# Performance work log

Hardware: AMD Instinct MI355X
Metric: run time of the kernel (lower is better)

The kernel has to match this reference:

```python
import jax, jax.numpy as jnp
import numpy as np

NUM_EXPERTS = 8
TOP_K = 2
BALANCE_LOSS_COEF = 0.01


def setup_inputs() -> dict:
    key = jax.random.key(0)
    ks = jax.random.split(key, 5)
    B, S, H, I, E = 8, 2048, 512, 2048, NUM_EXPERTS
    return {
        "hidden_states": jax.random.normal(ks[0], (B, S, H), dtype=jnp.float32),
        "Wg": jax.random.normal(ks[1], (H, E), dtype=jnp.float32) * (1.0 / np.sqrt(H)),
        "bg": jnp.zeros((E,), dtype=jnp.float32),
        "W1": jax.random.normal(ks[2], (E, H, I), dtype=jnp.float32) * (1.0 / np.sqrt(H)),
        "b1": jnp.zeros((E, I), dtype=jnp.float32),
        "W2": jax.random.normal(ks[3], (E, I, H), dtype=jnp.float32) * (1.0 / np.sqrt(I)),
        "b2": jnp.zeros((E, H), dtype=jnp.float32),
    }


def reference(hidden_states, Wg, bg, W1, b1, W2, b2):
    B, S, H = hidden_states.shape
    E, K = NUM_EXPERTS, TOP_K

    # ---- Router: softmax gate + top-k, renormalized weights ----
    logits = jnp.einsum('bsh,he->bse', hidden_states, Wg) + bg       # [B,S,E]
    probs = jax.nn.softmax(logits, axis=-1)                          # [B,S,E]
    top_p, top_i = jax.lax.top_k(probs, K)                           # [B,S,K]
    routing_weights = top_p / jnp.sum(top_p, axis=-1, keepdims=True)  # [B,S,K]

    # ---- Experts: compute every expert densely (small fixed E), then gather ----
    h = jnp.einsum('bsh,ehi->ebsi', hidden_states, W1) + b1[:, None, None, :]
    h = jax.nn.gelu(h)
    y = jnp.einsum('ebsi,eih->ebsh', h, W2) + b2[:, None, None, :]   # [E,B,S,H]

    y = jnp.moveaxis(y, 0, 2)                                        # [B,S,E,H]
    sel = jnp.take_along_axis(y, top_i[..., None], axis=2)           # [B,S,K,H]
    output = jnp.sum(routing_weights[..., None] * sel, axis=2) + hidden_states

    # ---- Load balancing loss (Switch-style): E * sum_e f_e * P_e ----
    assign = jnp.sum(jax.nn.one_hot(top_i, E, dtype=probs.dtype), axis=2)  # [B,S,E]
    f = jnp.mean(assign, axis=(0, 1)) / K                            # fraction dispatched
    P = jnp.mean(probs, axis=(0, 1))                                 # mean router prob
    balance_loss = BALANCE_LOSS_COEF * E * jnp.sum(f * P)

    return output, balance_loss
```

## Files before the change

kernel.cpp:

```cpp
#include <hip/hip_runtime.h>

#define BS_TOK 16384
#define HD 512
#define IDIM 2048
#define NE 8
#define RT_MAX 264
#define CAP (RT_MAX * 128)

typedef unsigned short u16;
typedef unsigned int u32;
typedef __attribute__((ext_vector_type(8))) __bf16 bf16x8;
typedef __attribute__((ext_vector_type(4))) float f32x4;

__device__ __forceinline__ u16 f2bf(float f) {
  u32 u = __builtin_bit_cast(u32, f);
  u += 0x7fffu + ((u >> 16) & 1u);
  return (u16)(u >> 16);
}
__device__ __forceinline__ float bflo(u32 u) { return __builtin_bit_cast(float, u << 16); }
__device__ __forceinline__ float bfhi(u32 u) { return __builtin_bit_cast(float, u & 0xffff0000u); }
__device__ __forceinline__ float gelu_t(float v) {
  float c = 0.7978845608028654f * (v + 0.044715f * v * v * v);
  return v / (1.0f + __expf(-2.0f * c));
}
__device__ __forceinline__ void gload16(const u16* g, u16* l) {
  __builtin_amdgcn_global_load_lds((const __attribute__((address_space(1))) u16*)g,
                                   (__attribute__((address_space(3))) u16*)l, 16, 0, 0);
}

__global__ void k_init(u32* counts, u32* pos, float* Psum, int* perm_t, float* perm_w) {
  int i = blockIdx.x * 256 + threadIdx.x;
  if (i < NE) { counts[i] = 0; pos[i] = 0; Psum[i] = 0.f; }
  if (i < CAP) { perm_t[i] = 0; perm_w[i] = 0.f; }
}

__global__ void k_transpose2(const float* __restrict__ W1, u16* __restrict__ W1T,
                             const float* __restrict__ W2, u16* __restrict__ W2T) {
  __shared__ float t[32][33];
  int z = blockIdx.z;
  const float* in; u16* out; int R, C, bx, by;
  if (z < NE) { in = W1; out = W1T; R = HD; C = IDIM; bx = blockIdx.x; by = blockIdx.y; }
  else { in = W2; out = W2T; R = IDIM; C = HD; bx = blockIdx.y; by = blockIdx.x; z -= NE; }
  size_t eb = (size_t)z * HD * IDIM;
  int c0 = bx * 32, r0 = by * 32;
  int tx = threadIdx.x, ty = threadIdx.y;
  #pragma unroll
  for (int j = ty; j < 32; j += 8) t[j][tx] = in[eb + (size_t)(r0 + j) * C + (c0 + tx)];
  __syncthreads();
  #pragma unroll
  for (int j = ty; j < 32; j += 8) out[eb + (size_t)(c0 + j) * R + (r0 + tx)] = f2bf(t[tx][j]);
}

__global__ void k_router(const float* __restrict__ x, const float* __restrict__ Wg,
                         const float* __restrict__ bg, int* __restrict__ top_e,
                         float* __restrict__ top_w, u32* __restrict__ counts,
                         float* __restrict__ Psum, u16* __restrict__ xb) {
  __shared__ float wg_s[HD * NE];
  __shared__ float Pp[NE];
  __shared__ u32 cnt[NE];
  int tid = threadIdx.x;
  if (tid < NE) { Pp[tid] = 0.f; cnt[tid] = 0; }
  for (int i = tid; i < HD * NE; i += 256) wg_s[i] = Wg[i];
  __syncthreads();
  int wv = tid >> 6, lane = tid & 63;
  int t = blockIdx.x * 4 + wv;
  const float4* xr = (const float4*)(x + (size_t)t * HD + lane * 8);
  float4 a = xr[0], b = xr[1];
  u32 p0 = f2bf(a.x) | ((u32)f2bf(a.y) << 16);
  u32 p1 = f2bf(a.z) | ((u32)f2bf(a.w) << 16);
  u32 p2 = f2bf(b.x) | ((u32)f2bf(b.y) << 16);
  u32 p3 = f2bf(b.z) | ((u32)f2bf(b.w) << 16);
  ((uint4*)(xb + (size_t)t * HD))[lane] = make_uint4(p0, p1, p2, p3);

  float acc[NE];
  #pragma unroll
  for (int e = 0; e < NE; ++e) acc[e] = 0.f;
  #pragma unroll
  for (int j = 0; j < 8; ++j) {
    float xv = j < 4 ? (&a.x)[j] : (&b.x)[j - 4];
    int h = lane * 8 + j;
    #pragma unroll
    for (int e = 0; e < NE; ++e) acc[e] += xv * wg_s[h * NE + e];
  }
  #pragma unroll
  for (int off = 32; off > 0; off >>= 1) {
    #pragma unroll
    for (int e = 0; e < NE; ++e) acc[e] += __shfl_down(acc[e], off);
  }
  if (lane == 0) {
    float lg[NE];
    #pragma unroll
    for (int e = 0; e < NE; ++e) lg[e] = acc[e] + bg[e];
    int i1 = 0; float m1 = lg[0];
    #pragma unroll
    for (int e = 1; e < NE; ++e) if (lg[e] > m1) { m1 = lg[e]; i1 = e; }
    int i2 = -1; float m2 = -1e30f;
    #pragma unroll
    for (int e = 0; e < NE; ++e) if (e != i1 && lg[e] > m2) { m2 = lg[e]; i2 = e; }
    float s = 0.f, p[NE];
    #pragma unroll
    for (int e = 0; e < NE; ++e) { p[e] = __expf(lg[e] - m1); s += p[e]; }
    float inv = 1.f / s;
    #pragma unroll
    for (int e = 0; e < NE; ++e) { p[e] *= inv; atomicAdd(&Pp[e], p[e]); }
    float denom = p[i1] + p[i2];
    top_e[2 * t] = i1; top_e[2 * t + 1] = i2;
    top_w[2 * t] = p[i1] / denom; top_w[2 * t + 1] = p[i2] / denom;
    atomicAdd(&cnt[i1], 1u); atomicAdd(&cnt[i2], 1u);
  }
  __syncthreads();
  if (tid < NE) { atomicAdd(&counts[tid], cnt[tid]); atomicAdd(&Psum[tid], Pp[tid]); }
}

__global__ void k_scan(const u32* __restrict__ counts, const float* __restrict__ Psum,
                       u32* __restrict__ padoff, u32* __restrict__ pos, float* __restrict__ out) {
  if (threadIdx.x == 0) {
    u32 off = 0; float loss = 0.f;
    for (int e = 0; e < NE; ++e) {
      padoff[e] = off; pos[e] = off;
      off += ((counts[e] + 127u) / 128u) * 128u;
      loss += ((float)counts[e] / (float)(BS_TOK * 2)) * (Psum[e] / (float)BS_TOK);
    }
    padoff[NE] = off;
    out[(size_t)BS_TOK * HD] = 0.01f * (float)NE * loss;
  }
}

__global__ void k_scatter(const int* __restrict__ top_e, const float* __restrict__ top_w,
                          u32* __restrict__ pos, int* __restrict__ perm_t,
                          float* __restrict__ perm_w, int* __restrict__ inv) {
  int g = blockIdx.x * 256 + threadIdx.x;
  int e = top_e[g]; float wgt = top_w[g];
  int lane = threadIdx.x & 63;
  #pragma unroll
  for (int ee = 0; ee < NE; ++ee) {
    unsigned long long m = __ballot(e == ee);
    if (e == ee) {
      int nb = __popcll(m & ((1ull << lane) - 1ull));
      int leader = __ffsll((unsigned long long)m) - 1;
      u32 base = 0;
      if (lane == leader) base = atomicAdd(&pos[ee], (u32)__popcll(m));
      base = __shfl(base, leader);
      int slot = (int)base + nb;
      perm_t[slot] = g >> 1;
      perm_w[slot] = wgt;
      inv[g] = slot;
    }
  }
}

__global__ void k_outinit(const float* __restrict__ x, float* __restrict__ out) {
  size_t i = (size_t)blockIdx.x * 256 + threadIdx.x;
  ((float4*)out)[i] = ((const float4*)x)[i];
}

template <int KSTEPS, int NCT, int NTOT, bool GATHER, bool ACT, bool ATOMIC>
__global__ __launch_bounds__(256, 2) void k_gemm(
    const u16* __restrict__ A, int lda, const u16* __restrict__ W,
    const float* __restrict__ bias, const int* __restrict__ perm_t,
    const float* __restrict__ perm_w, const u32* __restrict__ padoff,
    u16* __restrict__ C, float* __restrict__ outA, int rt0) {
  __shared__ u16 As[2][8192], Bs[2][8192];
  int nb = gridDim.x;
  int b = blockIdx.x;
  int tile = (b & 7) * (nb >> 3) + (b >> 3);
  int rt = rt0 + tile / NCT, ct = tile % NCT;
  u32 s0 = (u32)rt * 128u;
  if (rt >= RT_MAX || s0 >= padoff[NE]) return;
  int e = 0;
  #pragma unroll
  for (int k = 1; k < NE; ++k) e += (s0 >= padoff[k]) ? 1 : 0;

  int tid = threadIdx.x;
  int wv = tid >> 6, lane = tid & 63;
  int l15 = lane & 15, lg4 = lane >> 4;
  int wr = wv >> 1, wc = wv & 1;

  int srow = tid >> 3;
  int cb = (tid & 7) * 16;
  int cbs = (cb ^ ((srow & 7) << 4)) >> 1;

  const u16* ap[4]; const u16* bp[4];
  #pragma unroll
  for (int i = 0; i < 4; ++i) {
    int r = i * 32 + srow;
    int arow = GATHER ? perm_t[s0 + r] : (int)(s0 + r);
    ap[i] = A + (size_t)arow * lda + cbs;
    bp[i] = W + ((size_t)e * NTOT + ct * 128 + r) * (KSTEPS * 64) + cbs;
  }

  f32x4 acc[4][4] = {};

  #pragma unroll
  for (int i = 0; i < 4; ++i) gload16(ap[i], As[0] + tid * 8 + i * 2048);
  #pragma unroll
  for (int i = 0; i < 4; ++i) gload16(bp[i], Bs[0] + tid * 8 + i * 2048);
  #pragma unroll
  for (int i = 0; i < 4; ++i) gload16(ap[i] + 64, As[1] + tid * 8 + i * 2048);
  #pragma unroll
  for (int i = 0; i < 4; ++i) gload16(bp[i] + 64, Bs[1] + tid * 8 + i * 2048);
  asm volatile("s_waitcnt vmcnt(8)" ::: "memory");
  __builtin_amdgcn_sched_barrier(0);
  __builtin_amdgcn_s_barrier();

  for (int ks = 0; ks < KSTEPS; ++ks) {
    int cur = ks & 1;
    const u16* Ab = As[cur];
    const u16* Bb = Bs[cur];
    bf16x8 af[2][4], bf[2][4];
    #pragma unroll
    for (int kk = 0; kk < 2; ++kk) {
      #pragma unroll
      for (int f = 0; f < 4; ++f) {
        int ra = wr * 64 + f * 16 + l15;
        af[kk][f] = *(const bf16x8*)((const char*)Ab +
                    (ra * 128 + ((kk * 64 + lg4 * 16) ^ ((ra & 7) << 4))));
        int rb = wc * 64 + f * 16 + l15;
        bf[kk][f] = *(const bf16x8*)((const char*)Bb +
                    (rb * 128 + ((kk * 64 + lg4 * 16) ^ ((rb & 7) << 4))));
      }
    }
    asm volatile("s_waitcnt lgkmcnt(0)" ::: "memory");
    __builtin_amdgcn_sched_barrier(0);
    __builtin_amdgcn_s_barrier();

    if (ks + 2 < KSTEPS) {
      int k0 = (ks + 2) * 64;
      #pragma unroll
      for (int i = 0; i < 4; ++i) gload16(ap[i] + k0, As[cur] + tid * 8 + i * 2048);
      #pragma unroll
      for (int i = 0; i < 4; ++i) gload16(bp[i] + k0, Bs[cur] + tid * 8 + i * 2048);
    }

    __builtin_amdgcn_s_setprio(1);
    #pragma unroll
    for (int kk = 0; kk < 2; ++kk) {
      #pragma unroll
      for (int i = 0; i < 4; ++i)
        #pragma unroll
        for (int j = 0; j < 4; ++j)
          acc[i][j] = __builtin_amdgcn_mfma_f32_16x16x32_bf16(af[kk][i], bf[kk][j], acc[i][j], 0, 0, 0);
    }
    __builtin_amdgcn_s_setprio(0);

    if (ks + 1 < KSTEPS) {
      if (ks + 2 < KSTEPS) {
        asm volatile("s_waitcnt vmcnt(8)" ::: "memory");
      } else {
        asm volatile("s_waitcnt vmcnt(0)" ::: "memory");
      }
      __builtin_amdgcn_sched_barrier(0);
      __builtin_amdgcn_s_barrier();
    }
  }

  int base_n = ct * 128 + wc * 64;
  float bv[4];
  #pragma unroll
  for (int j = 0; j < 4; ++j) bv[j] = bias[e * NTOT + base_n + j * 16 + l15];

  #pragma unroll
  for (int i = 0; i < 4; ++i) {
    u32 mrow = s0 + wr * 64 + i * 16 + lg4 * 4;
    #pragma unroll
    for (int rr = 0; rr < 4; ++rr) {
      u32 m = mrow + rr;
      if (ATOMIC) {
        int tok = perm_t[m]; float wt = perm_w[m];
        if (wt != 0.f) {
          #pragma unroll
          for (int j = 0; j < 4; ++j) {
            float v = (acc[i][j][rr] + bv[j]) * wt;
            atomicAdd(outA + (size_t)tok * HD + base_n + j * 16 + l15, v);
          }
        }
      } else {
        #pragma unroll
        for (int j = 0; j < 4; ++j) {
          float v = acc[i][j][rr] + bv[j];
          if (ACT) v = gelu_t(v);
          C[(size_t)m * NTOT + base_n + j * 16 + l15] = f2bf(v);
        }
      }
    }
  }
}

__global__ void k_final(const float* __restrict__ x, const u16* __restrict__ y,
                        const int* __restrict__ inv, const float* __restrict__ top_w,
                        float* __restrict__ out) {
  int tid = threadIdx.x;
  int t = blockIdx.x * 4 + (tid >> 6);
  int lane = tid & 63;
  int s0 = inv[2 * t], s1 = inv[2 * t + 1];
  float w0 = top_w[2 * t], w1 = top_w[2 * t + 1];
  size_t xo = (size_t)t * HD + lane * 8;
  float4 a = *(const float4*)(x + xo);
  float4 b = *(const float4*)(x + xo + 4);
  uint4 ya = *(const uint4*)(y + (size_t)s0 * HD + lane * 8);
  uint4 yb = *(const uint4*)(y + (size_t)s1 * HD + lane * 8);
  float4 o0, o1;
  o0.x = a.x + w0 * bflo(ya.x) + w1 * bflo(yb.x);
  o0.y = a.y + w0 * bfhi(ya.x) + w1 * bfhi(yb.x);
  o0.z = a.z + w0 * bflo(ya.y) + w1 * bflo(yb.y);
  o0.w = a.w + w0 * bfhi(ya.y) + w1 * bfhi(yb.y);
  o1.x = b.x + w0 * bflo(ya.z) + w1 * bflo(yb.z);
  o1.y = b.y + w0 * bfhi(ya.z) + w1 * bfhi(yb.z);
  o1.z = b.z + w0 * bflo(ya.w) + w1 * bflo(yb.w);
  o1.w = b.w + w0 * bfhi(ya.w) + w1 * bfhi(yb.w);
  *(float4*)(out + xo) = o0;
  *(float4*)(out + xo + 4) = o1;
}

extern "C" void kernel_launch(void* const* d_in, const int* in_sizes, int n_in,
                              void* d_out, int out_size, void* d_ws, size_t ws_size,
                              hipStream_t stream) {
  const float* x  = (const float*)d_in[0];
  const float* Wg = (const float*)d_in[1];
  const float* bg = (const float*)d_in[2];
  const float* W1 = (const float*)d_in[3];
  const float* b1 = (const float*)d_in[4];
  const float* W2 = (const float*)d_in[5];
  const float* b2 = (const float*)d_in[6];
  float* out = (float*)d_out;

  char* w = (char*)d_ws;
  u32* counts  = (u32*)(w + 0);
  u32* pos     = (u32*)(w + 32);
  float* Psum  = (float*)(w + 64);
  u32* padoff  = (u32*)(w + 96);
  int* top_e   = (int*)(w + 256);
  float* top_w = (float*)(w + 256 + 131072);
  int* invm    = (int*)(w + 256 + 2 * 131072);
  int* perm_t  = (int*)(w + 256 + 3 * 131072);
  float* perm_w = (float*)(w + 256 + 3 * 131072 + 135168);
  u16* xb  = (u16*)(w + 663808);
  u16* W1T = (u16*)(w + 17441024);
  u16* W2T = (u16*)(w + 34218240);
  u16* h   = (u16*)(w + 50995456);
  u16* y   = (u16*)(w + 189407488);

  bool modeA = ws_size >= 224010496ull;
  int T;
  if (modeA) {
    T = RT_MAX;
  } else {
    size_t hspace = ws_size > 50995456ull ? ws_size - 50995456ull : 0;
    T = (int)(hspace / (128ull * IDIM * 2));
    T &= ~1;
    if (T < 2) return;
    if (T > RT_MAX) T = RT_MAX;
  }

  k_init<<<(CAP + 255) / 256, 256, 0, stream>>>(counts, pos, Psum, perm_t, perm_w);
  k_transpose2<<<dim3(IDIM / 32, HD / 32, 2 * NE), dim3(32, 8), 0, stream>>>(W1, W1T, W2, W2T);
  k_router<<<BS_TOK / 4, 256, 0, stream>>>(x, Wg, bg, top_e, top_w, counts, Psum, xb);
  k_scan<<<1, 64, 0, stream>>>(counts, Psum, padoff, pos, out);
  k_scatter<<<(BS_TOK * 2) / 256, 256, 0, stream>>>(top_e, top_w, pos, perm_t, perm_w, invm);
  if (!modeA) k_outinit<<<(BS_TOK * HD / 4) / 256, 256, 0, stream>>>(x, out);

  int nch = (RT_MAX + T - 1) / T;
  for (int c = 0; c < nch; ++c) {
    int rt0 = c * T;
    u16* hadj = h - (size_t)rt0 * 128 * IDIM;
    k_gemm<8, 16, IDIM, true, true, false><<<T * 16, 256, 0, stream>>>(
        xb, HD, W1T, b1, perm_t, perm_w, padoff, hadj, nullptr, rt0);
    if (modeA) {
      k_gemm<32, 4, HD, false, false, false><<<T * 4, 256, 0, stream>>>(
          hadj, IDIM, W2T, b2, perm_t, perm_w, padoff, y, nullptr, rt0);
    } else {
      k_gemm<32, 4, HD, false, false, true><<<T * 4, 256, 0, stream>>>(
          hadj, IDIM, W2T, b2, perm_t, perm_w, padoff, nullptr, out, rt0);
    }
  }
  if (modeA) k_final<<<BS_TOK / 4, 256, 0, stream>>>(x, y, invm, top_w, out);
}
```

Measured before the change: 380.2 us.

## Use hardware bf16 convert, exp2-based GELU, bias-initialized accumulators, memset init

Replaces the software round-to-nearest bf16 conversion with the v_cvt_pk_bf16_f32 instruction in the weight transpose and GEMM epilogue. GELU is rewritten with a folded-constant exp2 and a hardware reciprocal. The bias is loaded into the accumulators before the K loop, so the epilogue no longer adds it. The k_init kernel is replaced by two hipMemsetAsync calls. Together these trim epilogue ALU work and one kernel launch, at some risk to rounding behaviour and to memset offsets matching the workspace layout.

```diff
diff --git a/kernel.cpp b/kernel.cpp
--- a/kernel.cpp
+++ b/kernel.cpp
@@ -17,21 +17,20 @@
   u += 0x7fffu + ((u >> 16) & 1u);
   return (u16)(u >> 16);
 }
+__device__ __forceinline__ u16 f2bf_hw(float f) {
+  u32 r;
+  asm("v_cvt_pk_bf16_f32 %0, %1, %2" : "=v"(r) : "v"(f), "v"(f));
+  return (u16)r;
+}
 __device__ __forceinline__ float bflo(u32 u) { return __builtin_bit_cast(float, u << 16); }
 __device__ __forceinline__ float bfhi(u32 u) { return __builtin_bit_cast(float, u & 0xffff0000u); }
 __device__ __forceinline__ float gelu_t(float v) {
-  float c = 0.7978845608028654f * (v + 0.044715f * v * v * v);
-  return v / (1.0f + __expf(-2.0f * c));
+  float t = v * (-2.302558f - 0.1029474f * v * v);
+  return v * __builtin_amdgcn_rcpf(1.0f + __builtin_amdgcn_exp2f(t));
 }
 __device__ __forceinline__ void gload16(const u16* g, u16* l) {
   __builtin_amdgcn_global_load_lds((const __attribute__((address_space(1))) u16*)g,
                                    (__attribute__((address_space(3))) u16*)l, 16, 0, 0);
-}
-
-__global__ void k_init(u32* counts, u32* pos, float* Psum, int* perm_t, float* perm_w) {
-  int i = blockIdx.x * 256 + threadIdx.x;
-  if (i < NE) { counts[i] = 0; pos[i] = 0; Psum[i] = 0.f; }
-  if (i < CAP) { perm_t[i] = 0; perm_w[i] = 0.f; }
 }
 
 __global__ void k_transpose2(const float* __restrict__ W1, u16* __restrict__ W1T,
@@ -48,7 +47,7 @@
   for (int j = ty; j < 32; j += 8) t[j][tx] = in[eb + (size_t)(r0 + j) * C + (c0 + tx)];
   __syncthreads();
   #pragma unroll
-  for (int j = ty; j < 32; j += 8) out[eb + (size_t)(c0 + j) * R + (r0 + tx)] = f2bf(t[tx][j]);
+  for (int j = ty; j < 32; j += 8) out[eb + (size_t)(c0 + j) * R + (r0 + tx)] = f2bf_hw(t[tx][j]);
 }
 
 __global__ void k_router(const float* __restrict__ x, const float* __restrict__ Wg,
@@ -189,7 +188,14 @@
     bp[i] = W + ((size_t)e * NTOT + ct * 128 + r) * (KSTEPS * 64) + cbs;
   }
 
-  f32x4 acc[4][4] = {};
+  int base_n = ct * 128 + wc * 64;
+  f32x4 acc[4][4];
+  #pragma unroll
+  for (int j = 0; j < 4; ++j) {
+    float bv = bias[e * NTOT + base_n + j * 16 + l15];
+    #pragma unroll
+    for (int i = 0; i < 4; ++i) acc[i][j] = f32x4{bv, bv, bv, bv};
+  }
 
   #pragma unroll
   for (int i = 0; i < 4; ++i) gload16(ap[i], As[0] + tid * 8 + i * 2048);
@@ -254,11 +260,6 @@
     }
   }
 
-  int base_n = ct * 128 + wc * 64;
-  float bv[4];
-  #pragma unroll
-  for (int j = 0; j < 4; ++j) bv[j] = bias[e * NTOT + base_n + j * 16 + l15];
-
   #pragma unroll
   for (int i = 0; i < 4; ++i) {
     u32 mrow = s0 + wr * 64 + i * 16 + lg4 * 4;
@@ -270,16 +271,16 @@
         if (wt != 0.f) {
           #pragma unroll
           for (int j = 0; j < 4; ++j) {
-            float v = (acc[i][j][rr] + bv[j]) * wt;
+            float v = acc[i][j][rr] * wt;
             atomicAdd(outA + (size_t)tok * HD + base_n + j * 16 + l15, v);
           }
         }
       } else {
         #pragma unroll
         for (int j = 0; j < 4; ++j) {
-          float v = acc[i][j][rr] + bv[j];
+          float v = acc[i][j][rr];
           if (ACT) v = gelu_t(v);
-          C[(size_t)m * NTOT + base_n + j * 16 + l15] = f2bf(v);
+          C[(size_t)m * NTOT + base_n + j * 16 + l15] = f2bf_hw(v);
         }
       }
     }
@@ -352,7 +353,8 @@
     if (T > RT_MAX) T = RT_MAX;
   }
 
-  k_init<<<(CAP + 255) / 256, 256, 0, stream>>>(counts, pos, Psum, perm_t, perm_w);
+  (void)hipMemsetAsync(w, 0, 256, stream);
+  (void)hipMemsetAsync(w + 393472, 0, 270336, stream);
   k_transpose2<<<dim3(IDIM / 32, HD / 32, 2 * NE), dim3(32, 8), 0, stream>>>(W1, W1T, W2, W2T);
   k_router<<<BS_TOK / 4, 256, 0, stream>>>(x, Wg, bg, top_e, top_w, counts, Psum, xb);
   k_scan<<<1, 64, 0, stream>>>(counts, Psum, padoff, pos, out);
```

Measured after the change: 364.7 us. 1.04x faster.
